# Performance work log

Hardware: AMD Instinct MI355X
Metric: run time of the kernel (lower is better)

Reference implementation:

```python
import jax, jax.numpy as jnp
import numpy as np

T, IN, H, CTX_LEN, CTXD, A = 256, 512, 1024, 200, 512, 512


def setup_inputs() -> dict:
    key = jax.random.key(0)
    ks = jax.random.split(key, 24)

    def w(k, shape, scale=0.02):
        return jax.random.normal(k, shape, dtype=jnp.float32) * scale

    r = jax.random.randint(ks[4], (T,), 0, T)
    # parent of node t must be an already-produced node (< t); t=0 unused (zeros fed)
    parent_t = r % jnp.maximum(jnp.arange(T), 1)

    return {
        "X": jax.random.normal(ks[0], (T, IN), jnp.float32),
        "context": jax.random.normal(ks[1], (CTX_LEN, CTXD), jnp.float32),
        "h0": jax.random.normal(ks[2], (H,), jnp.float32),
        "c0": jax.random.normal(ks[3], (H,), jnp.float32),
        "parent_t": parent_t,
        # fused gate weights, column blocks in (i, f, c, o) order
        "Wx": w(ks[5], (IN, 4 * H)),   # wi/wf/wc/wo
        "Uh": w(ks[6], (H, 4 * H)),    # ui/uf/uc/uo
        "Cc": w(ks[7], (CTXD, 4 * H)), # ci/cf/cc/co
        "Ph": w(ks[8], (H, 4 * H)),    # pi/pf/pc/po
        "Hh": w(ks[9], (H, 4 * H)),    # hi/hf/hc/ho
        "b4": w(ks[10], (4 * H,)),     # biases of wi/wf/wc/wo
        # context attention
        "Wctx": w(ks[11], (CTXD, A)),
        "bctx": w(ks[12], (A,)),
        "Wh": w(ks[13], (H, A)),
        "v": w(ks[14], (A,)),
        "bv": w(ks[15], ()),
        # history attention
        "Whist": w(ks[16], (H, A)),
        "bhist": w(ks[17], (A,)),
        "Whh": w(ks[18], (H, A)),
        "v2": w(ks[19], (A,)),
        "bv2": w(ks[20], ()),
    }


def reference(X, context, h0, c0, parent_t, Wx, Uh, Cc, Ph, Hh, b4,
              Wctx, bctx, Wh, v, bv, Whist, bhist, Whh, v2, bv2):
    Tn, Hd = X.shape[0], h0.shape[0]
    # loop-invariant half of the context attention (att_ctx(context))
    ctx_trans = context @ Wctx + bctx                  # [L, A]
    hist_init = jnp.zeros((Tn, Hd), X.dtype)           # growing history buffer
    ts = jnp.arange(Tn)

    def step(carry, xs):
        h, hist = carry
        t, x_t, p_t = xs
        # --- attention over source context ---
        e = jnp.tanh(ctx_trans + h @ Wh) @ v + bv      # [L]
        alpha = jax.nn.softmax(e)
        ctx_vec = alpha @ context                      # [CTXD]
        # --- attention over decoding history (nodes j < t) ---
        he = jnp.tanh(hist @ Whist + bhist + h @ Whh) @ v2 + bv2   # [T]
        he = jnp.where(ts < t, he, -1e9)
        h_ctx = jnp.where(t > 0, jax.nn.softmax(he) @ hist, 0.0)   # [H]
        # --- parent hidden state feed (zeros at t == 0) ---
        par_h = jnp.where(t > 0, hist[p_t], 0.0)       # [H]
        # --- fused gates ---
        z = x_t @ Wx + h @ Uh + ctx_vec @ Cc + par_h @ Ph + h_ctx @ Hh + b4
        zi, zf, zc, zo = jnp.split(z, 4)
        # NOTE: faithful to source — forward_node returns the OLD c, so the
        # cell state used each step stays c0 forever.
        c_new = jax.nn.sigmoid(zf) * c0 + jax.nn.sigmoid(zi) * jnp.tanh(zc)
        h_new = jax.nn.sigmoid(zo) * jnp.tanh(c_new)
        hist = hist.at[t].set(h_new)
        return (h_new, hist), (h_new, ctx_vec)

    _, (out_h, out_ctx) = jax.lax.scan(step, (h0, hist_init), (ts, X, parent_t))
    return out_h, out_ctx
```

## Files before the change

### kernel.cpp

```cpp
#include <hip/hip_runtime.h>

#define T_STEPS 256
#define H_DIM   1024
#define L_CTX   200
#define CTXD    512
#define A_DIM   512
#define G4      4096
#define KT2     3072
#define NBLK    64
#define NTHR    512

typedef __attribute__((ext_vector_type(8))) unsigned short us8;

#define OFF_XWB    0
#define OFF_CTXW   (OFF_XWB   + T_STEPS*G4)
#define OFF_HIST   (OFF_CTXW  + L_CTX*A_DIM)
#define OFF_UW     (OFF_HIST  + T_STEPS*H_DIM)
#define OFF_E      (OFF_UW    + T_STEPS*H_DIM)
#define OFF_HISTW  (OFF_E     + T_STEPS*A_DIM)
#define OFF_CC     (OFF_HISTW + T_STEPS*A_DIM)
#define OFF_HH     (OFF_CC    + G4*L_CTX/2)
#define OFF_W4TI8  (OFF_HH    + G4*T_STEPS/2)
#define OFF_WSC    (OFF_W4TI8 + G4*KT2/4)
#define OFF_WT3    (OFF_WSC   + G4)
#define OFF_BAR    (OFF_WT3   + 1536*H_DIM/2)
#define WS_FLOATS  (OFF_BAR   + 256)

__device__ __forceinline__ float sigmoidf_(float x) { return 1.f / (1.f + __expf(-x)); }
__device__ __forceinline__ float bf2f(unsigned short h) { return __uint_as_float((unsigned)h << 16); }
__device__ __forceinline__ unsigned short f2bf(float x) {
    unsigned u = __float_as_uint(x);
    return (unsigned short)((u + 0x7FFFu + ((u >> 16) & 1u)) >> 16);
}
__device__ __forceinline__ void st_ag(float* p, float v) {
    __hip_atomic_store(p, v, __ATOMIC_RELAXED, __HIP_MEMORY_SCOPE_AGENT);
}
__device__ __forceinline__ float wred(float x) {
    #pragma unroll
    for (int off = 32; off; off >>= 1) x += __shfl_down(x, off);
    return x;
}
__device__ __forceinline__ float wredmax(float x) {
    #pragma unroll
    for (int off = 32; off; off >>= 1) x = fmaxf(x, __shfl_down(x, off));
    return x;
}

__device__ __forceinline__ void gbar(unsigned char* bar, int b, unsigned ph) {
    __syncthreads();
    if (threadIdx.x < 64) {
        const unsigned char tgt = (unsigned char)ph;
        if (threadIdx.x == 0)
            __hip_atomic_store(bar + b, tgt, __ATOMIC_RELAXED, __HIP_MEMORY_SCOPE_AGENT);
        for (int spins = 0; spins < 40000; ++spins) {
            unsigned char f = __hip_atomic_load(bar + threadIdx.x, __ATOMIC_RELAXED,
                                                __HIP_MEMORY_SCOPE_AGENT);
            if (!__any((int)(signed char)(f - tgt) < 0)) break;
            __builtin_amdgcn_s_sleep(1);
        }
    }
    __syncthreads();
}


__global__ __launch_bounds__(256) void k_xwb(const float* __restrict__ X,
                                             const float* __restrict__ Wx,
                                             const float* __restrict__ b4,
                                             float* __restrict__ XWb) {
    int c  = blockIdx.x * 256 + threadIdx.x;
    int r0 = blockIdx.y * 8;
    float acc[8] = {0,0,0,0,0,0,0,0};
    for (int k = 0; k < 512; ++k) {
        float wv = Wx[(size_t)k * G4 + c];
        #pragma unroll
        for (int r = 0; r < 8; ++r) acc[r] += X[(r0 + r) * 512 + k] * wv;
    }
    float bb = b4[c];
    #pragma unroll
    for (int r = 0; r < 8; ++r) XWb[(size_t)(r0 + r) * G4 + c] = acc[r] + bb;
}

__global__ __launch_bounds__(256) void k_ctxw(const float* __restrict__ ctx,
                                              const float* __restrict__ Wctx,
                                              const float* __restrict__ bctx,
                                              float* __restrict__ ctxW) {
    int a  = blockIdx.x * 256 + threadIdx.x;
    int l0 = blockIdx.y * 8;
    float acc[8] = {0,0,0,0,0,0,0,0};
    for (int k = 0; k < 512; ++k) {
        float wv = Wctx[(size_t)k * A_DIM + a];
        #pragma unroll
        for (int r = 0; r < 8; ++r) acc[r] += ctx[(l0 + r) * CTXD + k] * wv;
    }
    float bb = bctx[a];
    #pragma unroll
    for (int r = 0; r < 8; ++r) ctxW[(l0 + r) * A_DIM + a] = acc[r] + bb;
}

__global__ __launch_bounds__(256) void k_cc(const float* __restrict__ ctx,
                                            const float* __restrict__ Cc,
                                            unsigned short* __restrict__ CCp) {
    int c  = blockIdx.x * 256 + threadIdx.x;
    int l0 = blockIdx.y * 8;
    float acc[8] = {0,0,0,0,0,0,0,0};
    for (int k = 0; k < 512; ++k) {
        float wv = Cc[(size_t)k * G4 + c];
        #pragma unroll
        for (int r = 0; r < 8; ++r) acc[r] += ctx[(l0 + r) * CTXD + k] * wv;
    }
    int colp = 4 * (c & 1023) + (c >> 10);
    #pragma unroll
    for (int r = 0; r < 8; ++r) CCp[(size_t)colp * L_CTX + l0 + r] = f2bf(acc[r]);
}

__global__ __launch_bounds__(256) void k_colmax(const float* __restrict__ Uh,
                                                const float* __restrict__ Ph,
                                                const float* __restrict__ Hh,
                                                float* __restrict__ wsc) {
    int c = blockIdx.x * 256 + threadIdx.x;
    float m = 0.f;
    for (int k = 0; k < 1024; ++k) {
        m = fmaxf(m, fabsf(Uh[(size_t)k * G4 + c]));
        m = fmaxf(m, fabsf(Ph[(size_t)k * G4 + c]));
        m = fmaxf(m, fabsf(Hh[(size_t)k * G4 + c]));
    }
    int colp = 4 * (c & 1023) + (c >> 10);
    wsc[colp] = fmaxf(m, 1e-20f) / 127.f;
}

__global__ __launch_bounds__(256) void k_packW4i8(const float* __restrict__ Uh,
                                                  const float* __restrict__ Ph,
                                                  const float* __restrict__ Hh,
                                                  const float* __restrict__ wsc,
                                                  signed char* __restrict__ W8) {
    __shared__ float tile[32][33];
    const int k0 = blockIdx.x * 32, d0 = blockIdx.y * 32, q = blockIdx.z;
    const int x = threadIdx.x & 31, yy = threadIdx.x >> 5;
    const int c = q * 1024 + d0 + x;
    #pragma unroll
    for (int i = 0; i < 32; i += 8) {
        int ka = k0 + yy + i;
        const float* src; int kk;
        if (ka < 1024)      { src = Uh; kk = ka; }
        else if (ka < 2048) { src = Ph; kk = ka - 1024; }
        else                { src = Hh; kk = ka - 2048; }
        tile[yy + i][x] = src[(size_t)kk * G4 + c];
    }
    __syncthreads();
    #pragma unroll
    for (int i = 0; i < 32; i += 8) {
        int dd = yy + i;
        int col = 4 * (d0 + dd) + q;
        float r = 1.f / wsc[col];
        float qv = rintf(tile[x][dd] * r);
        qv = fminf(fmaxf(qv, -127.f), 127.f);
        W8[(size_t)col * KT2 + k0 + x] = (signed char)qv;
    }
}

__global__ __launch_bounds__(256) void k_packW3(const float* __restrict__ Wh,
                                                const float* __restrict__ Whh,
                                                const float* __restrict__ Whist,
                                                unsigned short* __restrict__ WT3) {
    __shared__ float tile[32][33];
    const int k0 = blockIdx.x * 32, c0 = blockIdx.y * 32, s = blockIdx.z;
    const float* S = (s == 0) ? Wh : (s == 1) ? Whh : Whist;
    const int x = threadIdx.x & 31, yy = threadIdx.x >> 5;
    #pragma unroll
    for (int i = 0; i < 32; i += 8)
        tile[yy + i][x] = S[(size_t)(k0 + yy + i) * 512 + c0 + x];
    __syncthreads();
    #pragma unroll
    for (int i = 0; i < 32; i += 8) {
        int dd = yy + i;
        WT3[(size_t)(s * 512 + c0 + dd) * H_DIM + k0 + x] = f2bf(tile[x][dd]);
    }
}


struct LP {
    const float *ctx, *c0, *v, *v2, *bv, *bv2, *bhist, *h0;
    const int* parent;
    float* ws;
    float* out;
};

__global__ __launch_bounds__(NTHR) void lstm_loop(LP p) {
    const int b    = blockIdx.x;
    const int tid  = threadIdx.x;
    const int lane = tid & 63, wv = tid >> 6;

    float* XWb   = p.ws + OFF_XWB;
    float* ctxW  = p.ws + OFF_CTXW;
    float* hist  = p.ws + OFF_HIST;
    float* UW    = p.ws + OFF_UW;
    float* E     = p.ws + OFF_E;
    float* histW = p.ws + OFF_HISTW;
    const unsigned short* CCp = (const unsigned short*)(p.ws + OFF_CC);
    unsigned short*       HHp = (unsigned short*)(p.ws + OFF_HH);
    const unsigned char*  W4I = (const unsigned char*)(p.ws + OFF_W4TI8);
    const float*          WSC = p.ws + OFF_WSC;
    const unsigned short* WT3 = (const unsigned short*)(p.ws + OFF_WT3);
    unsigned char* bar = (unsigned char*)(p.ws + OFF_BAR);

    __shared__ float xs[2048];
    __shared__ float uw_[512];
    __shared__ float vs_[512], v2s_[512];
    __shared__ float aC[256], aH[256];
    __shared__ float red[16], sc[4], zs[64];

    vs_[tid] = p.v[tid];  v2s_[tid] = p.v2[tid];
    xs[tid] = p.h0[tid];  xs[512 + tid] = p.h0[512 + tid];
    xs[1024 + tid] = 0.f; xs[1536 + tid] = 0.f;
    __syncthreads();

    #pragma unroll
    for (int rr = 0; rr < 2; ++rr) {
        int j = b * 16 + wv * 2 + rr;
        const us8* wr = (const us8*)(WT3 + (size_t)j * H_DIM) + lane * 2;
        us8 a0 = wr[0], a1 = wr[1];
        float s = 0.f;
        #pragma unroll
        for (int k = 0; k < 8; ++k) s += bf2f(a0[k]) * xs[lane * 16 + k];
        #pragma unroll
        for (int k = 0; k < 8; ++k) s += bf2f(a1[k]) * xs[lane * 16 + 8 + k];
        s = wred(s);
        if (lane == 0)
            st_ag(UW + j, (j < A_DIM) ? s : s + p.bhist[j - A_DIM]);
    }
    unsigned ph = 1;
    gbar(bar, b, ph++);

    const int cg  = tid >> 3;
    const int sub = tid & 7;
    const uint2* Wcol = (const uint2*)(W4I + (size_t)(b * 64 + cg) * KT2);
    const float  wscl = WSC[b * 64 + cg];
    const unsigned short* ccC = CCp + (size_t)(b * 64 + cg) * L_CTX;
    unsigned short*       hhC = HHp + (size_t)(b * 64 + cg) * T_STEPS;

    for (int t = 0; t < T_STEPS; ++t) {
        if (b < 25) {
            uw_[tid] = UW[(size_t)t * H_DIM + tid];
            __syncthreads();
            const int idx = b * 8 + wv;
            if (idx < L_CTX) {
                const float4* cw = (const float4*)(ctxW + (size_t)idx * A_DIM) + lane * 2;
                float4 c0v = cw[0], c1v = cw[1];
                const int i0 = lane * 8;
                float e = tanhf(c0v.x + uw_[i0+0]) * vs_[i0+0]
                        + tanhf(c0v.y + uw_[i0+1]) * vs_[i0+1]
                        + tanhf(c0v.z + uw_[i0+2]) * vs_[i0+2]
                        + tanhf(c0v.w + uw_[i0+3]) * vs_[i0+3]
                        + tanhf(c1v.x + uw_[i0+4]) * vs_[i0+4]
                        + tanhf(c1v.y + uw_[i0+5]) * vs_[i0+5]
                        + tanhf(c1v.z + uw_[i0+6]) * vs_[i0+6]
                        + tanhf(c1v.w + uw_[i0+7]) * vs_[i0+7];
                e = wred(e);
                if (lane == 0) st_ag(E + (size_t)t * A_DIM + idx, e + p.bv[0]);
            }
        } else if (b >= 32) {
            uw_[tid] = UW[(size_t)t * H_DIM + 512 + tid];
            __syncthreads();
            const int j = (b - 32) * 8 + wv;
            if (j < t) {
                const float4* hw4 = (const float4*)(histW + (size_t)j * A_DIM) + lane * 2;
                float4 h0v = hw4[0], h1v = hw4[1];
                const int i0 = lane * 8;
                float e = tanhf(h0v.x + uw_[i0+0]) * v2s_[i0+0]
                        + tanhf(h0v.y + uw_[i0+1]) * v2s_[i0+1]
                        + tanhf(h0v.z + uw_[i0+2]) * v2s_[i0+2]
                        + tanhf(h0v.w + uw_[i0+3]) * v2s_[i0+3]
                        + tanhf(h1v.x + uw_[i0+4]) * v2s_[i0+4]
                        + tanhf(h1v.y + uw_[i0+5]) * v2s_[i0+5]
                        + tanhf(h1v.z + uw_[i0+6]) * v2s_[i0+6]
                        + tanhf(h1v.w + uw_[i0+7]) * v2s_[i0+7];
                e = wred(e);
                if (lane == 0) st_ag(E + (size_t)t * A_DIM + 256 + j, e + p.bv2[0]);
            }
        }
        gbar(bar, b, ph++);

        if (tid < L_CTX) aC[tid] = E[(size_t)t * A_DIM + tid];
        if (tid < t)     aH[tid] = E[(size_t)t * A_DIM + 256 + tid];
        __syncthreads();
        {
            float pC = (tid < L_CTX) ? aC[tid] : -3e38f;
            float pH = (tid < t)     ? aH[tid] : -3e38f;
            pC = wredmax(pC); pH = wredmax(pH);
            if (lane == 0) { red[wv] = pC; red[8 + wv] = pH; }
            __syncthreads();
            if (tid == 0) { float m = -3e38f; for (int g = 0; g < 8; ++g) m = fmaxf(m, red[g]); sc[0] = m; }
            if (tid == 1) { float m = -3e38f; for (int g = 0; g < 8; ++g) m = fmaxf(m, red[8 + g]); sc[1] = m; }
            __syncthreads();
            const float mC = sc[0], mH = sc[1];
            float sCp = 0.f, sHp = 0.f;
            if (tid < L_CTX) { float x = __expf(aC[tid] - mC); aC[tid] = x; sCp = x; }
            if (tid < t)     { float x = __expf(aH[tid] - mH); aH[tid] = x; sHp = x; }
            sCp = wred(sCp); sHp = wred(sHp);
            if (lane == 0) { red[wv] = sCp; red[8 + wv] = sHp; }
            __syncthreads();
            if (tid == 0) { float s = 0.f; for (int g = 0; g < 8; ++g) s += red[g]; sc[2] = s; }
            if (tid == 1) { float s = 0.f; for (int g = 0; g < 8; ++g) s += red[8 + g]; sc[3] = s; }
            __syncthreads();
            const float rC = 1.f / sc[2];
            const float rH = (t > 0) ? 1.f / sc[3] : 0.f;

            float g0 = 0.f, g1 = 0.f;
            #pragma unroll 8
            for (int i = 0; i < 32; ++i) {
                const int c = i * 8 + sub;
                uint2 w = Wcol[c];
                const float* xk = xs + c * 8;
                int wa = (int)w.x, wb = (int)w.y;
                float d0 = (float)((wa << 24) >> 24) * xk[0]
                         + (float)((wa << 16) >> 24) * xk[1]
                         + (float)((wa <<  8) >> 24) * xk[2]
                         + (float)( wa        >> 24) * xk[3];
                float d1 = (float)((wb << 24) >> 24) * xk[4]
                         + (float)((wb << 16) >> 24) * xk[5]
                         + (float)((wb <<  8) >> 24) * xk[6]
                         + (float)( wb        >> 24) * xk[7];
                if (i & 1) g1 += d0 + d1; else g0 += d0 + d1;
            }
            float acc = (g0 + g1) * wscl;
            float attc = 0.f, atth = 0.f;
            for (int l = sub; l < L_CTX; l += 8) attc += aC[l] * bf2f(ccC[l]);
            for (int j = sub; j < t; j += 8)     atth += aH[j] * bf2f(hhC[j]);
            acc += attc * rC + atth * rH;
            acc += __shfl_down(acc, 4, 8);
            acc += __shfl_down(acc, 2, 8);
            acc += __shfl_down(acc, 1, 8);
            if (sub == 0) zs[cg] = acc;
            __syncthreads();
            if (tid < 16) {
                const int d = b * 16 + tid;
                float zi = zs[4 * tid + 0] + XWb[(size_t)t * G4 + 0 * 1024 + d];
                float zf = zs[4 * tid + 1] + XWb[(size_t)t * G4 + 1 * 1024 + d];
                float zc = zs[4 * tid + 2] + XWb[(size_t)t * G4 + 2 * 1024 + d];
                float zo = zs[4 * tid + 3] + XWb[(size_t)t * G4 + 3 * 1024 + d];
                float cn = sigmoidf_(zf) * p.c0[d] + sigmoidf_(zi) * tanhf(zc);
                float hn = sigmoidf_(zo) * tanhf(cn);
                st_ag(hist + (size_t)t * H_DIM + d, hn);
                p.out[(size_t)t * H_DIM + d] = hn;
            }
            {
                const int d = b * 8 + wv;
                float s = 0.f;
                for (int l = lane; l < L_CTX; l += 64)
                    s += aC[l] * p.ctx[(size_t)l * CTXD + d];
                s = wred(s);
                if (lane == 0)
                    p.out[(size_t)T_STEPS * H_DIM + (size_t)t * CTXD + d] = s * rC;
            }
        }
        gbar(bar, b, ph++);

        if (t == T_STEPS - 1) break;

        xs[tid]       = hist[(size_t)t * H_DIM + tid];
        xs[512 + tid] = hist[(size_t)t * H_DIM + 512 + tid];
        {
            const int ptn = p.parent[t + 1];
            xs[1024 + tid] = hist[(size_t)ptn * H_DIM + tid];
            xs[1536 + tid] = hist[(size_t)ptn * H_DIM + 512 + tid];
        }
        __syncthreads();
        {
            #pragma unroll
            for (int rr = 0; rr < 3; ++rr) {
                const int j = b * 24 + wv * 3 + rr;
                const us8* wr = (const us8*)(WT3 + (size_t)j * H_DIM) + lane * 2;
                us8 a0 = wr[0], a1 = wr[1];
                float s = 0.f;
                #pragma unroll
                for (int k = 0; k < 8; ++k) s += bf2f(a0[k]) * xs[lane * 16 + k];
                #pragma unroll
                for (int k = 0; k < 8; ++k) s += bf2f(a1[k]) * xs[lane * 16 + 8 + k];
                s = wred(s);
                if (lane == 0) {
                    if (j < A_DIM)          st_ag(UW + (size_t)(t + 1) * H_DIM + j, s);
                    else if (j < 2 * A_DIM) st_ag(UW + (size_t)(t + 1) * H_DIM + j, s + p.bhist[j - A_DIM]);
                    else                    st_ag(histW + (size_t)t * A_DIM + (j - 2 * A_DIM), s);
                }
            }
            float g0 = 0.f, g1 = 0.f;
            #pragma unroll 8
            for (int i = 0; i < 16; ++i) {
                const int c2 = 256 + i * 8 + sub;
                uint2 w = Wcol[c2];
                const float* xk = xs + (c2 - 256) * 8;
                int wa = (int)w.x, wb = (int)w.y;
                float d0 = (float)((wa << 24) >> 24) * xk[0]
                         + (float)((wa << 16) >> 24) * xk[1]
                         + (float)((wa <<  8) >> 24) * xk[2]
                         + (float)( wa        >> 24) * xk[3];
                float d1 = (float)((wb << 24) >> 24) * xk[4]
                         + (float)((wb << 16) >> 24) * xk[5]
                         + (float)((wb <<  8) >> 24) * xk[6]
                         + (float)( wb        >> 24) * xk[7];
                if (i & 1) g1 += d0 + d1; else g0 += d0 + d1;
            }
            float hv = (g0 + g1) * wscl;
            hv += __shfl_down(hv, 4, 8);
            hv += __shfl_down(hv, 2, 8);
            hv += __shfl_down(hv, 1, 8);
            if (sub == 0) hhC[t] = f2bf(hv);
        }
        gbar(bar, b, ph++);
    }
}


extern "C" void kernel_launch(void* const* d_in, const int* in_sizes, int n_in,
                              void* d_out, int out_size, void* d_ws, size_t ws_size,
                              hipStream_t stream) {
    if (ws_size < (size_t)WS_FLOATS * sizeof(float)) return;

    const float* X      = (const float*)d_in[0];
    const float* ctx    = (const float*)d_in[1];
    const float* h0     = (const float*)d_in[2];
    const float* c0     = (const float*)d_in[3];
    const int*   parent = (const int*)  d_in[4];
    const float* Wx     = (const float*)d_in[5];
    const float* Uh     = (const float*)d_in[6];
    const float* Cc     = (const float*)d_in[7];
    const float* Ph     = (const float*)d_in[8];
    const float* Hh     = (const float*)d_in[9];
    const float* b4     = (const float*)d_in[10];
    const float* Wctx   = (const float*)d_in[11];
    const float* bctx   = (const float*)d_in[12];
    const float* Wh     = (const float*)d_in[13];
    const float* v      = (const float*)d_in[14];
    const float* bv     = (const float*)d_in[15];
    const float* Whist  = (const float*)d_in[16];
    const float* bhist  = (const float*)d_in[17];
    const float* Whh    = (const float*)d_in[18];
    const float* v2     = (const float*)d_in[19];
    const float* bv2    = (const float*)d_in[20];
    float* ws  = (float*)d_ws;
    float* out = (float*)d_out;

    hipMemsetAsync((char*)d_ws + (size_t)OFF_BAR * sizeof(float), 0, 1024, stream);

    hipLaunchKernelGGL(k_xwb,      dim3(16, 32),    dim3(256), 0, stream, X,   Wx,   b4,   ws + OFF_XWB);
    hipLaunchKernelGGL(k_ctxw,     dim3(2, 25),     dim3(256), 0, stream, ctx, Wctx, bctx, ws + OFF_CTXW);
    hipLaunchKernelGGL(k_cc,       dim3(16, 25),    dim3(256), 0, stream, ctx, Cc,
                       (unsigned short*)(ws + OFF_CC));
    hipLaunchKernelGGL(k_colmax,   dim3(16),        dim3(256), 0, stream, Uh, Ph, Hh, ws + OFF_WSC);
    hipLaunchKernelGGL(k_packW4i8, dim3(96, 32, 4), dim3(256), 0, stream, Uh, Ph, Hh,
                       ws + OFF_WSC, (signed char*)(ws + OFF_W4TI8));
    hipLaunchKernelGGL(k_packW3,   dim3(32, 16, 3), dim3(256), 0, stream, Wh, Whh, Whist,
                       (unsigned short*)(ws + OFF_WT3));

    LP p{ctx, c0, v, v2, bv, bv2, bhist, h0, parent, ws, out};
    hipLaunchKernelGGL(lstm_loop, dim3(NBLK), dim3(NTHR), 0, stream, p);
}
```

Baseline: 7.569 ms.

## Spread attention scores over all blocks and overlap int8 gate matvec with scoring

Measured after the change: 7.711 ms. No clear change (+1.9%).

```diff
diff --git a/kernel.cpp b/kernel.cpp
--- a/kernel.cpp
+++ b/kernel.cpp
@@ -52,11 +52,10 @@
         const unsigned char tgt = (unsigned char)ph;
         if (threadIdx.x == 0)
             __hip_atomic_store(bar + b, tgt, __ATOMIC_RELAXED, __HIP_MEMORY_SCOPE_AGENT);
-        for (int spins = 0; spins < 40000; ++spins) {
+        for (int spins = 0; spins < 30000; ++spins) {
             unsigned char f = __hip_atomic_load(bar + threadIdx.x, __ATOMIC_RELAXED,
                                                 __HIP_MEMORY_SCOPE_AGENT);
             if (!__any((int)(signed char)(f - tgt) < 0)) break;
-            __builtin_amdgcn_s_sleep(1);
         }
     }
     __syncthreads();
@@ -204,14 +203,15 @@
     unsigned char* bar = (unsigned char*)(p.ws + OFF_BAR);
 
     __shared__ float xs[2048];
-    __shared__ float uw_[512];
+    __shared__ float uwA[1024];
     __shared__ float vs_[512], v2s_[512];
     __shared__ float aC[256], aH[256];
-    __shared__ float red[16], sc[4], zs[64];
+    __shared__ float red[16], sc[4], zs1[64], zs[64];
 
     vs_[tid] = p.v[tid];  v2s_[tid] = p.v2[tid];
     xs[tid] = p.h0[tid];  xs[512 + tid] = p.h0[512 + tid];
     xs[1024 + tid] = 0.f; xs[1536 + tid] = 0.f;
+    const float bv = p.bv[0], bv2 = p.bv2[0];
     __syncthreads();
 
     #pragma unroll
@@ -231,52 +231,74 @@
     unsigned ph = 1;
     gbar(bar, b, ph++);
 
-    const int cg  = tid >> 3;
+    const int grp = tid >> 3;
     const int sub = tid & 7;
-    const uint2* Wcol = (const uint2*)(W4I + (size_t)(b * 64 + cg) * KT2);
-    const float  wscl = WSC[b * 64 + cg];
-    const unsigned short* ccC = CCp + (size_t)(b * 64 + cg) * L_CTX;
-    unsigned short*       hhC = HHp + (size_t)(b * 64 + cg) * T_STEPS;
+    const uint2* Wcol = (const uint2*)(W4I + (size_t)(b * 64 + grp) * KT2);
+    const float  wscl = WSC[b * 64 + grp];
+    const unsigned short* ccC = CCp + (size_t)(b * 64 + grp) * L_CTX;
+    unsigned short*       hhC = HHp + (size_t)(b * 64 + grp) * T_STEPS;
 
     for (int t = 0; t < T_STEPS; ++t) {
-        if (b < 25) {
-            uw_[tid] = UW[(size_t)t * H_DIM + tid];
-            __syncthreads();
-            const int idx = b * 8 + wv;
-            if (idx < L_CTX) {
-                const float4* cw = (const float4*)(ctxW + (size_t)idx * A_DIM) + lane * 2;
-                float4 c0v = cw[0], c1v = cw[1];
-                const int i0 = lane * 8;
-                float e = tanhf(c0v.x + uw_[i0+0]) * vs_[i0+0]
-                        + tanhf(c0v.y + uw_[i0+1]) * vs_[i0+1]
-                        + tanhf(c0v.z + uw_[i0+2]) * vs_[i0+2]
-                        + tanhf(c0v.w + uw_[i0+3]) * vs_[i0+3]
-                        + tanhf(c1v.x + uw_[i0+4]) * vs_[i0+4]
-                        + tanhf(c1v.y + uw_[i0+5]) * vs_[i0+5]
-                        + tanhf(c1v.z + uw_[i0+6]) * vs_[i0+6]
-                        + tanhf(c1v.w + uw_[i0+7]) * vs_[i0+7];
-                e = wred(e);
-                if (lane == 0) st_ag(E + (size_t)t * A_DIM + idx, e + p.bv[0]);
-            }
-        } else if (b >= 32) {
-            uw_[tid] = UW[(size_t)t * H_DIM + 512 + tid];
-            __syncthreads();
-            const int j = (b - 32) * 8 + wv;
-            if (j < t) {
-                const float4* hw4 = (const float4*)(histW + (size_t)j * A_DIM) + lane * 2;
-                float4 h0v = hw4[0], h1v = hw4[1];
-                const int i0 = lane * 8;
-                float e = tanhf(h0v.x + uw_[i0+0]) * v2s_[i0+0]
-                        + tanhf(h0v.y + uw_[i0+1]) * v2s_[i0+1]
-                        + tanhf(h0v.z + uw_[i0+2]) * v2s_[i0+2]
-                        + tanhf(h0v.w + uw_[i0+3]) * v2s_[i0+3]
-                        + tanhf(h1v.x + uw_[i0+4]) * v2s_[i0+4]
-                        + tanhf(h1v.y + uw_[i0+5]) * v2s_[i0+5]
-                        + tanhf(h1v.z + uw_[i0+6]) * v2s_[i0+6]
-                        + tanhf(h1v.w + uw_[i0+7]) * v2s_[i0+7];
-                e = wred(e);
-                if (lane == 0) st_ag(E + (size_t)t * A_DIM + 256 + j, e + p.bv2[0]);
-            }
+        uwA[tid]       = UW[(size_t)t * H_DIM + tid];
+        uwA[512 + tid] = UW[(size_t)t * H_DIM + 512 + tid];
+        __syncthreads();
+        {
+            const int i0 = lane * 8;
+            if (wv < 4) {
+                const int idx = wv * 64 + b;
+                if (idx < L_CTX) {
+                    const float4* cw = (const float4*)(ctxW + (size_t)idx * A_DIM + i0);
+                    float4 ca = cw[0], cb = cw[1];
+                    float e = tanhf(ca.x + uwA[i0+0]) * vs_[i0+0]
+                            + tanhf(ca.y + uwA[i0+1]) * vs_[i0+1]
+                            + tanhf(ca.z + uwA[i0+2]) * vs_[i0+2]
+                            + tanhf(ca.w + uwA[i0+3]) * vs_[i0+3]
+                            + tanhf(cb.x + uwA[i0+4]) * vs_[i0+4]
+                            + tanhf(cb.y + uwA[i0+5]) * vs_[i0+5]
+                            + tanhf(cb.z + uwA[i0+6]) * vs_[i0+6]
+                            + tanhf(cb.w + uwA[i0+7]) * vs_[i0+7];
+                    e = wred(e);
+                    if (lane == 0) st_ag(E + (size_t)t * A_DIM + idx, e + bv);
+                }
+            } else {
+                const int j = (wv - 4) * 64 + b;
+                if (j < t) {
+                    const float4* hw4 = (const float4*)(histW + (size_t)j * A_DIM + i0);
+                    float4 ha = hw4[0], hb = hw4[1];
+                    float e = tanhf(ha.x + uwA[512+i0+0]) * v2s_[i0+0]
+                            + tanhf(ha.y + uwA[512+i0+1]) * v2s_[i0+1]
+                            + tanhf(ha.z + uwA[512+i0+2]) * v2s_[i0+2]
+                            + tanhf(ha.w + uwA[512+i0+3]) * v2s_[i0+3]
+                            + tanhf(hb.x + uwA[512+i0+4]) * v2s_[i0+4]
+                            + tanhf(hb.y + uwA[512+i0+5]) * v2s_[i0+5]
+                            + tanhf(hb.z + uwA[512+i0+6]) * v2s_[i0+6]
+                            + tanhf(hb.w + uwA[512+i0+7]) * v2s_[i0+7];
+                    e = wred(e);
+                    if (lane == 0) st_ag(E + (size_t)t * A_DIM + 256 + j, e + bv2);
+                }
+            }
+            float g0 = 0.f, g1 = 0.f;
+            #pragma unroll 8
+            for (int i = 0; i < 32; ++i) {
+                const int c = i * 8 + sub;
+                uint2 w = Wcol[c];
+                const float* xk = xs + c * 8;
+                int wa = (int)w.x, wb = (int)w.y;
+                float d0 = (float)((wa << 24) >> 24) * xk[0]
+                         + (float)((wa << 16) >> 24) * xk[1]
+                         + (float)((wa <<  8) >> 24) * xk[2]
+                         + (float)( wa        >> 24) * xk[3];
+                float d1 = (float)((wb << 24) >> 24) * xk[4]
+                         + (float)((wb << 16) >> 24) * xk[5]
+                         + (float)((wb <<  8) >> 24) * xk[6]
+                         + (float)( wb        >> 24) * xk[7];
+                if (i & 1) g1 += d0 + d1; else g0 += d0 + d1;
+            }
+            float zp = (g0 + g1) * wscl;
+            zp += __shfl_down(zp, 4, 8);
+            zp += __shfl_down(zp, 2, 8);
+            zp += __shfl_down(zp, 1, 8);
+            if (sub == 0) zs1[grp] = zp;
         }
         gbar(bar, b, ph++);
 
@@ -305,32 +327,14 @@
             const float rC = 1.f / sc[2];
             const float rH = (t > 0) ? 1.f / sc[3] : 0.f;
 
-            float g0 = 0.f, g1 = 0.f;
-            #pragma unroll 8
-            for (int i = 0; i < 32; ++i) {
-                const int c = i * 8 + sub;
-                uint2 w = Wcol[c];
-                const float* xk = xs + c * 8;
-                int wa = (int)w.x, wb = (int)w.y;
-                float d0 = (float)((wa << 24) >> 24) * xk[0]
-                         + (float)((wa << 16) >> 24) * xk[1]
-                         + (float)((wa <<  8) >> 24) * xk[2]
-                         + (float)( wa        >> 24) * xk[3];
-                float d1 = (float)((wb << 24) >> 24) * xk[4]
-                         + (float)((wb << 16) >> 24) * xk[5]
-                         + (float)((wb <<  8) >> 24) * xk[6]
-                         + (float)( wb        >> 24) * xk[7];
-                if (i & 1) g1 += d0 + d1; else g0 += d0 + d1;
-            }
-            float acc = (g0 + g1) * wscl;
             float attc = 0.f, atth = 0.f;
             for (int l = sub; l < L_CTX; l += 8) attc += aC[l] * bf2f(ccC[l]);
             for (int j = sub; j < t; j += 8)     atth += aH[j] * bf2f(hhC[j]);
-            acc += attc * rC + atth * rH;
-            acc += __shfl_down(acc, 4, 8);
-            acc += __shfl_down(acc, 2, 8);
-            acc += __shfl_down(acc, 1, 8);
-            if (sub == 0) zs[cg] = acc;
+            float attp = attc * rC + atth * rH;
+            attp += __shfl_down(attp, 4, 8);
+            attp += __shfl_down(attp, 2, 8);
+            attp += __shfl_down(attp, 1, 8);
+            if (sub == 0) zs[grp] = zs1[grp] + attp;
             __syncthreads();
             if (tid < 16) {
                 const int d = b * 16 + tid;
@@ -353,9 +357,8 @@
                     p.out[(size_t)T_STEPS * H_DIM + (size_t)t * CTXD + d] = s * rC;
             }
         }
+        if (t == T_STEPS - 1) break;
         gbar(bar, b, ph++);
-
-        if (t == T_STEPS - 1) break;
 
         xs[tid]       = hist[(size_t)t * H_DIM + tid];
         xs[512 + tid] = hist[(size_t)t * H_DIM + 512 + tid];
```
